# Performance work log

Hardware: AMD Instinct MI355X
Metric: run time of the kernel (lower is better)

The kernel has to match this reference:

```python
import jax, jax.numpy as jnp
import numpy as np

DIM = 1024
HEADS = 16
DHEAD = 64
INNER = HEADS * DHEAD
EPS = 1e-5


def layer_norm(x, g, b):
    mu = jnp.mean(x, axis=-1, keepdims=True)
    var = jnp.mean(jnp.square(x - mu), axis=-1, keepdims=True)
    return (x - mu) * jax.lax.rsqrt(var + EPS) * g + b


def apply_rope(x, cos, sin):
    # x: [b, h, s, d]; cos/sin broadcast as [1, 1, s, d/2]
    d2 = x.shape[-1] // 2
    x1, x2 = x[..., :d2], x[..., d2:]
    return jnp.concatenate([x1 * cos - x2 * sin, x2 * cos + x1 * sin], axis=-1)


def setup_inputs() -> dict:
    key = jax.random.key(0)
    ks = jax.random.split(key, 10)
    B, N, S = 8, 256, 4096
    latents = jax.random.normal(ks[0], (B, N, DIM), dtype=jnp.float32)
    context = jax.random.normal(ks[1], (B, S, DIM), dtype=jnp.float32)
    cos = jax.random.uniform(ks[2], (S, DHEAD // 2), dtype=jnp.float32)
    sin = jax.random.uniform(ks[3], (S, DHEAD // 2), dtype=jnp.float32)
    init = lambda k, shp, fan_in: jax.random.normal(k, shp, dtype=jnp.float32) / np.sqrt(fan_in)
    return {
        "latents": latents,
        "context": context,
        "cos": cos,
        "sin": sin,
        "ln_lat_g": jnp.ones((DIM,), jnp.float32),
        "ln_lat_b": jnp.zeros((DIM,), jnp.float32),
        "ln_ctx_g": jnp.ones((DIM,), jnp.float32),
        "ln_ctx_b": jnp.zeros((DIM,), jnp.float32),
        "Wq": init(ks[4], (DIM, INNER), DIM),
        "Wkv": init(ks[5], (DIM, 2 * INNER), DIM),
        "Wo": init(ks[6], (INNER, DIM), INNER),
        "bo": jnp.zeros((DIM,), jnp.float32),
    }


def reference(latents, context, cos, sin, ln_lat_g, ln_lat_b, ln_ctx_g, ln_ctx_b, Wq, Wkv, Wo, bo):
    b, n, _ = latents.shape
    s = context.shape[1]
    lat = layer_norm(latents, ln_lat_g, ln_lat_b)
    ctx = layer_norm(context, ln_ctx_g, ln_ctx_b)
    q = (lat @ Wq).reshape(b, n, HEADS, DHEAD).transpose(0, 2, 1, 3)   # [b,h,n,d]
    kv = ctx @ Wkv
    k, v = jnp.split(kv, 2, axis=-1)
    k = k.reshape(b, s, HEADS, DHEAD).transpose(0, 2, 1, 3)           # [b,h,s,d]
    v = v.reshape(b, s, HEADS, DHEAD).transpose(0, 2, 1, 3)
    k = apply_rope(k, cos[None, None], sin[None, None])
    scale = DHEAD ** (-0.5)
    attn = jnp.einsum('bhnd,bhsd->bhns', q, k) * scale
    attn = jnp.clip(attn, -11.0, 11.0)
    attn = jax.nn.softmax(attn, axis=-1)
    out = jnp.einsum('bhns,bhsd->bhnd', attn, v)
    out = out.transpose(0, 2, 1, 3).reshape(b, n, INNER)
    return out @ Wo + bo
```

## Files before the change

kernel.cpp:

```cpp
#include <hip/hip_runtime.h>
#include <hip/hip_bf16.h>
#include <math.h>

#define DIM   1024
#define HEADS 16
#define DHEAD 64
#define NB    8
#define NLAT  256
#define SCTX  4096

typedef short bf16x8 __attribute__((ext_vector_type(8)));
typedef float f32x4  __attribute__((ext_vector_type(4)));

__device__ __forceinline__ unsigned short f2b(float f) {
    union { float f; unsigned u; } x; x.f = f;
    unsigned r = x.u + 0x7FFFu + ((x.u >> 16) & 1u);
    return (unsigned short)(r >> 16);
}

__device__ __forceinline__ unsigned pkbf16(float a, float b) {
    float2 f2; f2.x = a; f2.y = b;
    __hip_bfloat162 h = __float22bfloat162_rn(f2);
    union { __hip_bfloat162 h; unsigned u; } cv; cv.h = h;
    return cv.u;
}

#define LN_WBLOCKS ((NB * NLAT + NB * SCTX) / 4)
__global__ __launch_bounds__(256) void prep_all(
    const float* __restrict__ latents, const float* __restrict__ context,
    const float* __restrict__ g_lat, const float* __restrict__ b_lat,
    const float* __restrict__ g_ctx, const float* __restrict__ b_ctx,
    const float* __restrict__ Wq, const float* __restrict__ Wkv,
    const float* __restrict__ Wo,
    unsigned short* __restrict__ lat_b, unsigned short* __restrict__ ctx_b,
    unsigned short* __restrict__ Wqb, unsigned short* __restrict__ Wkvb,
    unsigned short* __restrict__ Wob)
{
    int gb = blockIdx.x, t = threadIdx.x;
    if (gb < LN_WBLOCKS) {
        int wid = t >> 6, lane = t & 63;
        int row = gb * 4 + wid;
        const float* x; const float* g; const float* b; unsigned short* y; int r;
        if (row < NB * NLAT) { x = latents; g = g_lat; b = b_lat; y = lat_b; r = row; }
        else { x = context; g = g_ctx; b = b_ctx; y = ctx_b; r = row - NB * NLAT; }
        const float4* xr = (const float4*)(x + (size_t)r * DIM);
        float4 v[4];
        float s = 0.f, sq = 0.f;
        #pragma unroll
        for (int i = 0; i < 4; ++i) {
            v[i] = xr[lane + i * 64];
            s  += v[i].x + v[i].y + v[i].z + v[i].w;
            sq += v[i].x * v[i].x + v[i].y * v[i].y + v[i].z * v[i].z + v[i].w * v[i].w;
        }
        #pragma unroll
        for (int off = 32; off > 0; off >>= 1) {
            s  += __shfl_xor(s, off);
            sq += __shfl_xor(sq, off);
        }
        float mu = s * (1.0f / DIM);
        float rs = rsqrtf(sq * (1.0f / DIM) - mu * mu + 1e-5f);
        #pragma unroll
        for (int i = 0; i < 4; ++i) {
            float4 gg = ((const float4*)g)[lane + i * 64];
            float4 bb = ((const float4*)b)[lane + i * 64];
            ushort4 o;
            o.x = f2b((v[i].x - mu) * rs * gg.x + bb.x);
            o.y = f2b((v[i].y - mu) * rs * gg.y + bb.y);
            o.z = f2b((v[i].z - mu) * rs * gg.z + bb.z);
            o.w = f2b((v[i].w - mu) * rs * gg.w + bb.w);
            ((ushort4*)(y + (size_t)r * DIM))[lane + i * 64] = o;
        }
    } else {
        __shared__ unsigned short tile[32][33];
        int id = gb - LN_WBLOCKS;
        int z = id >> 10, y = (id >> 5) & 31, xb = id & 31;
        const float* W; unsigned short* Wt; int N, coloff = 0;
        switch (z) {
            case 0: W = Wq;  Wt = Wqb;  N = DIM;     break;
            case 1: W = Wkv; Wt = Wkvb; N = 2 * DIM; break;
            case 2: W = Wkv; Wt = Wkvb; N = 2 * DIM; coloff = DIM; break;
            default: W = Wo; Wt = Wob;  N = DIM;     break;
        }
        int n0 = xb * 32 + coloff, k0 = y * 32;
        int tx = t & 31, ty = t >> 5;
        #pragma unroll
        for (int i = 0; i < 4; ++i) {
            int k = k0 + ty + i * 8;
            tile[tx][ty + i * 8] = f2b(W[(size_t)k * N + n0 + tx]);
        }
        __syncthreads();
        #pragma unroll
        for (int i = 0; i < 4; ++i) {
            int n = n0 + ty + i * 8;
            Wt[(size_t)n * DIM + k0 + tx] = tile[ty + i * 8][tx];
        }
    }
}

__global__ __launch_bounds__(256, 2) void gemm_mfma(
    const unsigned short* __restrict__ A, const unsigned short* __restrict__ Bn,
    const unsigned short* __restrict__ Aq, const unsigned short* __restrict__ Bq,
    int K, const float* __restrict__ bias,
    const float* __restrict__ cosp, const float* __restrict__ sinp,
    float* __restrict__ outf,
    unsigned short* __restrict__ outk, unsigned short* __restrict__ outv,
    unsigned short* __restrict__ outq,
    int mode, int ldc)
{
    __shared__ __align__(16) unsigned short As[128 * 64];
    __shared__ __align__(16) unsigned short Bs[128 * 64];
    int t = threadIdx.x;
    int wave = t >> 6, lane = t & 63;
    int g = blockIdx.x;
    if (mode == 2) g += ldc;
    int m_tile, n_tile;
    if (mode == 2) {
        if (g >= 4096) {
            g -= 4096; mode = 1;
            A = Aq; Bn = Bq;
            n_tile = g & 7; m_tile = g >> 3;
        } else {
            int xcd = g & 7, j = g >> 3;
            int ngrp = j >> 8;
            n_tile = ngrp * 8 + (j & 7);
            m_tile = (xcd << 5) + ((j >> 3) & 31);
        }
    } else {
        n_tile = g & 7; m_tile = g >> 3;
    }
    int m_base = m_tile * 128, n_base = n_tile * 128;
    int wr = wave >> 1, wc = wave & 1;
    int quad = lane >> 4, ln = lane & 15;

    f32x4 zero = {0.f, 0.f, 0.f, 0.f};
    f32x4 acc[4][4];
    #pragma unroll
    for (int i = 0; i < 4; ++i)
        #pragma unroll
        for (int j = 0; j < 4; ++j) acc[i][j] = zero;

    const unsigned short* Ag = A  + (size_t)m_base * K;
    const unsigned short* Bg = Bn + (size_t)n_base * K;

    int srow  = lane >> 3;
    int schk  = ((lane & 7) ^ srow) * 8;

    for (int k0 = 0; k0 < K; k0 += 64) {
        __syncthreads();
        #pragma unroll
        for (int j = 0; j < 4; ++j) {
            int grp = j * 4 + wave;
            int row = grp * 8 + srow;
            __builtin_amdgcn_global_load_lds(
                (const __attribute__((address_space(1))) void*)(Ag + (size_t)row * K + k0 + schk),
                (__attribute__((address_space(3))) void*)(As + grp * 512 + lane * 8),
                16, 0, 0);
            __builtin_amdgcn_global_load_lds(
                (const __attribute__((address_space(1))) void*)(Bg + (size_t)row * K + k0 + schk),
                (__attribute__((address_space(3))) void*)(Bs + grp * 512 + lane * 8),
                16, 0, 0);
        }
        __syncthreads();
        #pragma unroll
        for (int kk = 0; kk < 2; ++kk) {
            bf16x8 af[4], bfr[4];
            int slot = ((kk * 4 + quad) ^ (ln & 7)) * 8;
            #pragma unroll
            for (int i = 0; i < 4; ++i) {
                af[i]  = *(const bf16x8*)(As + (wr * 64 + i * 16 + ln) * 64 + slot);
                bfr[i] = *(const bf16x8*)(Bs + (wc * 64 + i * 16 + ln) * 64 + slot);
            }
            #pragma unroll
            for (int i = 0; i < 4; ++i)
                #pragma unroll
                for (int j = 0; j < 4; ++j)
                    acc[i][j] = __builtin_amdgcn_mfma_f32_16x16x32_bf16(af[i], bfr[j], acc[i][j], 0, 0, 0);
        }
    }

    int cl = ln, rq = quad;
    if (mode == 2 && n_base >= DIM) {
        #pragma unroll
        for (int i = 0; i < 4; ++i) {
            int s0 = m_base + wr * 64 + i * 16 + rq * 4;
            int b  = s0 >> 12, s = s0 & 4095;
            #pragma unroll
            for (int j = 0; j < 4; ++j) {
                int n2 = n_base + wc * 64 + j * 16 + cl - DIM;
                int h = n2 >> 6, d = n2 & 63;
                ushort4 pk;
                pk.x = f2b(acc[i][j][0]); pk.y = f2b(acc[i][j][1]);
                pk.z = f2b(acc[i][j][2]); pk.w = f2b(acc[i][j][3]);
                *(ushort4*)(outv + (((size_t)(b * HEADS + h) * DHEAD + d) * SCTX) + s) = pk;
            }
        }
    } else if (mode == 2) {
        #pragma unroll
        for (int i = 0; i < 4; ++i) {
            #pragma unroll
            for (int r = 0; r < 4; ++r) {
                int m = m_base + wr * 64 + i * 16 + rq * 4 + r;
                int b = m >> 12, s = m & 4095;
                #pragma unroll
                for (int j = 0; j < 2; ++j) {
                    int n = n_base + wc * 64 + j * 16 + cl;
                    int h = n >> 6, d1 = n & 63;
                    float x1 = acc[i][j][r], x2 = acc[i][j + 2][r];
                    float c  = cosp[s * 32 + d1];
                    float sn = sinp[s * 32 + d1];
                    unsigned short* kr =
                        outk + (((size_t)(b * HEADS + h) * SCTX + s) * DHEAD) + d1;
                    kr[0]  = f2b(x1 * c - x2 * sn);
                    kr[32] = f2b(x2 * c + x1 * sn);
                }
            }
        }
    } else {
        #pragma unroll
        for (int i = 0; i < 4; ++i) {
            #pragma unroll
            for (int j = 0; j < 4; ++j) {
                #pragma unroll
                for (int r = 0; r < 4; ++r) {
                    int m = m_base + wr * 64 + i * 16 + rq * 4 + r;
                    int n = n_base + wc * 64 + j * 16 + cl;
                    float cv = acc[i][j][r];
                    if (mode == 0) {
                        outf[(size_t)m * ldc + n] = cv + bias[n];
                    } else {
                        int b = m >> 8, nn = m & 255;
                        int h = n >> 6, d = n & 63;
                        outq[(((size_t)(b * HEADS + h) * NLAT + nn) * DHEAD) + d] =
                            f2b(cv * 0.18033688f);
                    }
                }
            }
        }
    }
}

#define PPAD 72
#define CLIP2 15.8696454f

__global__ __launch_bounds__(256, 3) void attn_mfma(
    const unsigned short* __restrict__ qb,
    const unsigned short* __restrict__ kb,
    const unsigned short* __restrict__ vtb,
    float* __restrict__ accp,
    float* __restrict__ lp)
{
    __shared__ __align__(16) unsigned short Ks[2][64 * 64];
    __shared__ __align__(16) unsigned short Vs[2][64 * 64];
    __shared__ __align__(16) unsigned short Ps[4 * 32 * PPAD];

    int t = threadIdx.x, w = t >> 6, l = t & 63;
    int bx = blockIdx.x;
    int gg = ((bx >> 4) << 3) + (bx & 7);
    int qh = (bx >> 3) & 1;
    int bh = gg >> 2;
    int sh = gg & 3;
    int quad = l >> 4, ln = l & 15;
    int q0 = qh * 128 + w * 32;

    bf16x8 qf[2][2];
    const unsigned short* qbase = qb + ((size_t)bh * NLAT + q0) * DHEAD;
    #pragma unroll
    for (int qsub = 0; qsub < 2; ++qsub)
        #pragma unroll
        for (int kc = 0; kc < 2; ++kc)
            qf[qsub][kc] = *(const bf16x8*)(qbase + (qsub * 16 + ln) * DHEAD + kc * 32 + quad * 8);

    f32x4 acc[2][4];
    #pragma unroll
    for (int i = 0; i < 2; ++i)
        #pragma unroll
        for (int j = 0; j < 4; ++j) acc[i][j] = (f32x4){0.f, 0.f, 0.f, 0.f};
    float lacc[2] = {0.f, 0.f};

    const unsigned short* kgb = kb  + (size_t)bh * SCTX * DHEAD;
    const unsigned short* vgb = vtb + (size_t)bh * DHEAD * SCTX;
    unsigned short* Pw = Ps + w * 32 * PPAD;

    int srow8 = l >> 3;
    int csrc  = (l & 7) ^ srow8;

    auto STAGE = [&](int s0, int bi) {
        #pragma unroll
        for (int i = 0; i < 2; ++i) {
            int rbase = w * 8 + i * 32;
            int row = rbase + srow8;
            __builtin_amdgcn_global_load_lds(
                (const __attribute__((address_space(1))) void*)(kgb + (size_t)(s0 + row) * DHEAD + csrc * 8),
                (__attribute__((address_space(3))) void*)(&Ks[bi][rbase * 64] + (size_t)l * 8),
                16, 0, 0);
            __builtin_amdgcn_global_load_lds(
                (const __attribute__((address_space(1))) void*)(vgb + (size_t)row * SCTX + s0 + csrc * 8),
                (__attribute__((address_space(3))) void*)(&Vs[bi][rbase * 64] + (size_t)l * 8),
                16, 0, 0);
        }
    };

    const int s_begin = sh * 1024;
    const int NT = 1024 / 64;

    STAGE(s_begin, 0);
    __syncthreads();

    for (int it = 0; it < NT; ++it) {
        int buf = it & 1;
        if (it + 1 < NT)
            STAGE(s_begin + (it + 1) * 64, buf ^ 1);

        #pragma unroll
        for (int msub = 0; msub < 4; ++msub) {
            bf16x8 af[2];
            #pragma unroll
            for (int kc = 0; kc < 2; ++kc) {
                int sr = msub * 16 + ln;
                int ck = (4 * kc + quad) ^ (ln & 7);
                af[kc] = *(const bf16x8*)(&Ks[buf][sr * 64 + ck * 8]);
            }
            #pragma unroll
            for (int nsub = 0; nsub < 2; ++nsub) {
                f32x4 c = {0.f, 0.f, 0.f, 0.f};
                c = __builtin_amdgcn_mfma_f32_16x16x32_bf16(af[0], qf[nsub][0], c, 0, 0, 0);
                c = __builtin_amdgcn_mfma_f32_16x16x32_bf16(af[1], qf[nsub][1], c, 0, 0, 0);
                float p[4];
                #pragma unroll
                for (int r = 0; r < 4; ++r) {
                    float sc = __builtin_amdgcn_fmed3f(c[r], -CLIP2, CLIP2);
                    p[r] = __builtin_amdgcn_exp2f(sc - CLIP2);
                    lacc[nsub] += p[r];
                }
                uint2 pk;
                pk.x = pkbf16(p[0], p[1]);
                pk.y = pkbf16(p[2], p[3]);
                *(uint2*)(Pw + (nsub * 16 + ln) * PPAD + msub * 16 + quad * 4) = pk;
            }
        }
        #pragma unroll
        for (int kc = 0; kc < 2; ++kc) {
            bf16x8 pa[2];
            #pragma unroll
            for (int qsub = 0; qsub < 2; ++qsub)
                pa[qsub] = *(const bf16x8*)(Pw + (qsub * 16 + ln) * PPAD + kc * 32 + quad * 8);
            #pragma unroll
            for (int dsub = 0; dsub < 4; ++dsub) {
                int dr = dsub * 16 + ln;
                int ck = (4 * kc + quad) ^ (ln & 7);
                bf16x8 vb = *(const bf16x8*)(&Vs[buf][dr * 64 + ck * 8]);
                acc[0][dsub] = __builtin_amdgcn_mfma_f32_16x16x32_bf16(pa[0], vb, acc[0][dsub], 0, 0, 0);
                acc[1][dsub] = __builtin_amdgcn_mfma_f32_16x16x32_bf16(pa[1], vb, acc[1][dsub], 0, 0, 0);
            }
        }
        __syncthreads();
    }

    float* accs = accp + (size_t)sh * (NB * HEADS * NLAT * DHEAD);
    float* ls   = lp   + (size_t)sh * (NB * HEADS * NLAT);

    #pragma unroll
    for (int nsub = 0; nsub < 2; ++nsub) {
        float v = lacc[nsub];
        v += __shfl_xor(v, 16);
        v += __shfl_xor(v, 32);
        if (l < 16)
            ls[bh * NLAT + q0 + nsub * 16 + l] = v;
    }
    #pragma unroll
    for (int qsub = 0; qsub < 2; ++qsub)
        #pragma unroll
        for (int dsub = 0; dsub < 4; ++dsub)
            #pragma unroll
            for (int r = 0; r < 4; ++r) {
                int qg = q0 + qsub * 16 + quad * 4 + r;
                int dg = dsub * 16 + ln;
                accs[((size_t)bh * NLAT + qg) * DHEAD + dg] = acc[qsub][dsub][r];
            }
}

__global__ __launch_bounds__(256) void attn_finalize(
    const float* __restrict__ accp, const float* __restrict__ lp,
    unsigned short* __restrict__ aob)
{
    const int ACC = NB * HEADS * NLAT * DHEAD;
    const int LSZ = NB * HEADS * NLAT;
    int idx = blockIdx.x * 256 + threadIdx.x;
    int d = idx & 63;
    int rest = idx >> 6;
    int n = rest & 255, bh = rest >> 8;
    int b = bh >> 4, h = bh & 15;
    float a = accp[idx] + accp[idx + ACC] + accp[idx + 2 * ACC] + accp[idx + 3 * ACC];
    float l = lp[rest] + lp[rest + LSZ] + lp[rest + 2 * LSZ] + lp[rest + 3 * LSZ];
    aob[(((size_t)b * NLAT + n) * HEADS + h) * DHEAD + d] = f2b(a / l);
}

extern "C" void kernel_launch(void* const* d_in, const int* in_sizes, int n_in,
                              void* d_out, int out_size, void* d_ws, size_t ws_size,
                              hipStream_t stream) {
    const float* latents  = (const float*)d_in[0];
    const float* context  = (const float*)d_in[1];
    const float* cosp     = (const float*)d_in[2];
    const float* sinp     = (const float*)d_in[3];
    const float* ln_lat_g = (const float*)d_in[4];
    const float* ln_lat_b = (const float*)d_in[5];
    const float* ln_ctx_g = (const float*)d_in[6];
    const float* ln_ctx_b = (const float*)d_in[7];
    const float* Wq  = (const float*)d_in[8];
    const float* Wkv = (const float*)d_in[9];
    const float* Wo  = (const float*)d_in[10];
    const float* bo  = (const float*)d_in[11];
    float* out = (float*)d_out;

    char* base = (char*)d_ws;
    unsigned short* lat_b = (unsigned short*)(base + 0);
    unsigned short* ctx_b = (unsigned short*)(base + 4194304);
    unsigned short* Wqb   = (unsigned short*)(base + 71303168);
    unsigned short* Wkvb  = (unsigned short*)(base + 73400320);
    unsigned short* Wob   = (unsigned short*)(base + 77594624);
    unsigned short* q_b   = (unsigned short*)(base + 79691776);
    unsigned short* k_b   = (unsigned short*)(base + 83886080);
    unsigned short* vT_b  = (unsigned short*)(base + 150994944);
    float*          accp  = (float*)(base + 218103808);
    float*          lp    = (float*)(base + 251658240);
    unsigned short* aob   = (unsigned short*)(base + 252182528);

    hipLaunchKernelGGL(prep_all, dim3(LN_WBLOCKS + 4096), dim3(256), 0, stream,
                       latents, context, ln_lat_g, ln_lat_b, ln_ctx_g, ln_ctx_b,
                       Wq, Wkv, Wo, lat_b, ctx_b, Wqb, Wkvb, Wob);
    hipLaunchKernelGGL(gemm_mfma, dim3(1408), dim3(256), 0, stream,
                       ctx_b, Wkvb, lat_b, Wqb, DIM, (const float*)nullptr,
                       cosp, sinp,
                       (float*)nullptr, k_b, vT_b, q_b, 2, 0);
    hipLaunchKernelGGL(gemm_mfma, dim3(1408), dim3(256), 0, stream,
                       ctx_b, Wkvb, lat_b, Wqb, DIM, (const float*)nullptr,
                       cosp, sinp,
                       (float*)nullptr, k_b, vT_b, q_b, 2, 1408);
    hipLaunchKernelGGL(gemm_mfma, dim3(1408), dim3(256), 0, stream,
                       ctx_b, Wkvb, lat_b, Wqb, DIM, (const float*)nullptr,
                       cosp, sinp,
                       (float*)nullptr, k_b, vT_b, q_b, 2, 2816);
    hipLaunchKernelGGL(attn_mfma, dim3(NB * HEADS * 8), dim3(256), 0, stream,
                       q_b, k_b, vT_b, accp, lp);
    hipLaunchKernelGGL(attn_finalize, dim3(NB * HEADS * NLAT * DHEAD / 256), dim3(256), 0, stream,
                       accp, lp, aob);
    hipLaunchKernelGGL(gemm_mfma, dim3(128), dim3(256), 0, stream,
                       aob, Wob, (const unsigned short*)nullptr, (const unsigned short*)nullptr,
                       DIM, bo,
                       (const float*)nullptr, (const float*)nullptr,
                       out, (unsigned short*)nullptr, (unsigned short*)nullptr,
                       (unsigned short*)nullptr, 0, DIM);
}
```

Before: 507.5 us.

## Merge KV GEMM launches and process both query halves per attention block

The three split KV/Q projection GEMM launches become one launch of 4224 blocks, with a simpler XCD-aware tile mapping (16 n-tiles per m-group). The attention kernel now handles all 256 queries of a head/split in one block, so each K/V tile staged into LDS is reused across both query halves and total K/V global traffic is halved. The cost is twice the accumulator registers, with launch bounds lowered to 2 blocks per CU, and half as many attention blocks (512), which lowers parallelism.

```diff
diff --git a/kernel.cpp b/kernel.cpp
--- a/kernel.cpp
+++ b/kernel.cpp
@@ -112,7 +112,6 @@
     int t = threadIdx.x;
     int wave = t >> 6, lane = t & 63;
     int g = blockIdx.x;
-    if (mode == 2) g += ldc;
     int m_tile, n_tile;
     if (mode == 2) {
         if (g >= 4096) {
@@ -121,9 +120,8 @@
             n_tile = g & 7; m_tile = g >> 3;
         } else {
             int xcd = g & 7, j = g >> 3;
-            int ngrp = j >> 8;
-            n_tile = ngrp * 8 + (j & 7);
-            m_tile = (xcd << 5) + ((j >> 3) & 31);
+            n_tile = j & 15;
+            m_tile = (xcd << 5) + (j >> 4);
         }
     } else {
         n_tile = g & 7; m_tile = g >> 3;
@@ -242,7 +240,7 @@
 #define PPAD 72
 #define CLIP2 15.8696454f
 
-__global__ __launch_bounds__(256, 3) void attn_mfma(
+__global__ __launch_bounds__(256, 2) void attn_mfma(
     const unsigned short* __restrict__ qb,
     const unsigned short* __restrict__ kb,
     const unsigned short* __restrict__ vtb,
@@ -254,28 +252,30 @@
     __shared__ __align__(16) unsigned short Ps[4 * 32 * PPAD];
 
     int t = threadIdx.x, w = t >> 6, l = t & 63;
-    int bx = blockIdx.x;
-    int gg = ((bx >> 4) << 3) + (bx & 7);
-    int qh = (bx >> 3) & 1;
-    int bh = gg >> 2;
-    int sh = gg & 3;
+    int bh = blockIdx.x >> 2;
+    int sh = blockIdx.x & 3;
     int quad = l >> 4, ln = l & 15;
-    int q0 = qh * 128 + w * 32;
-
-    bf16x8 qf[2][2];
-    const unsigned short* qbase = qb + ((size_t)bh * NLAT + q0) * DHEAD;
+
+    bf16x8 qf[2][2][2];
     #pragma unroll
-    for (int qsub = 0; qsub < 2; ++qsub)
-        #pragma unroll
-        for (int kc = 0; kc < 2; ++kc)
-            qf[qsub][kc] = *(const bf16x8*)(qbase + (qsub * 16 + ln) * DHEAD + kc * 32 + quad * 8);
-
-    f32x4 acc[2][4];
+    for (int qblk = 0; qblk < 2; ++qblk) {
+        const unsigned short* qbase =
+            qb + ((size_t)bh * NLAT + qblk * 128 + w * 32) * DHEAD;
+        #pragma unroll
+        for (int qsub = 0; qsub < 2; ++qsub)
+            #pragma unroll
+            for (int kc = 0; kc < 2; ++kc)
+                qf[qblk][qsub][kc] = *(const bf16x8*)(qbase + (qsub * 16 + ln) * DHEAD + kc * 32 + quad * 8);
+    }
+
+    f32x4 acc[2][2][4];
     #pragma unroll
-    for (int i = 0; i < 2; ++i)
-        #pragma unroll
-        for (int j = 0; j < 4; ++j) acc[i][j] = (f32x4){0.f, 0.f, 0.f, 0.f};
-    float lacc[2] = {0.f, 0.f};
+    for (int qblk = 0; qblk < 2; ++qblk)
+        #pragma unroll
+        for (int i = 0; i < 2; ++i)
+            #pragma unroll
+            for (int j = 0; j < 4; ++j) acc[qblk][i][j] = (f32x4){0.f, 0.f, 0.f, 0.f};
+    float lacc[2][2] = {{0.f, 0.f}, {0.f, 0.f}};
 
     const unsigned short* kgb = kb  + (size_t)bh * SCTX * DHEAD;
     const unsigned short* vgb = vtb + (size_t)bh * DHEAD * SCTX;
@@ -312,45 +312,48 @@
             STAGE(s_begin + (it + 1) * 64, buf ^ 1);
 
         #pragma unroll
-        for (int msub = 0; msub < 4; ++msub) {
-            bf16x8 af[2];
+        for (int qblk = 0; qblk < 2; ++qblk) {
+            #pragma unroll
+            for (int msub = 0; msub < 4; ++msub) {
+                bf16x8 af[2];
+                #pragma unroll
+                for (int kc = 0; kc < 2; ++kc) {
+                    int sr = msub * 16 + ln;
+                    int ck = (4 * kc + quad) ^ (ln & 7);
+                    af[kc] = *(const bf16x8*)(&Ks[buf][sr * 64 + ck * 8]);
+                }
+                #pragma unroll
+                for (int nsub = 0; nsub < 2; ++nsub) {
+                    f32x4 c = {0.f, 0.f, 0.f, 0.f};
+                    c = __builtin_amdgcn_mfma_f32_16x16x32_bf16(af[0], qf[qblk][nsub][0], c, 0, 0, 0);
+                    c = __builtin_amdgcn_mfma_f32_16x16x32_bf16(af[1], qf[qblk][nsub][1], c, 0, 0, 0);
+                    float p[4];
+                    #pragma unroll
+                    for (int r = 0; r < 4; ++r) {
+                        float sc = __builtin_amdgcn_fmed3f(c[r], -CLIP2, CLIP2);
+                        p[r] = __builtin_amdgcn_exp2f(sc - CLIP2);
+                        lacc[qblk][nsub] += p[r];
+                    }
+                    uint2 pk;
+                    pk.x = pkbf16(p[0], p[1]);
+                    pk.y = pkbf16(p[2], p[3]);
+                    *(uint2*)(Pw + (nsub * 16 + ln) * PPAD + msub * 16 + quad * 4) = pk;
+                }
+            }
             #pragma unroll
             for (int kc = 0; kc < 2; ++kc) {
-                int sr = msub * 16 + ln;
-                int ck = (4 * kc + quad) ^ (ln & 7);
-                af[kc] = *(const bf16x8*)(&Ks[buf][sr * 64 + ck * 8]);
-            }
-            #pragma unroll
-            for (int nsub = 0; nsub < 2; ++nsub) {
-                f32x4 c = {0.f, 0.f, 0.f, 0.f};
-                c = __builtin_amdgcn_mfma_f32_16x16x32_bf16(af[0], qf[nsub][0], c, 0, 0, 0);
-                c = __builtin_amdgcn_mfma_f32_16x16x32_bf16(af[1], qf[nsub][1], c, 0, 0, 0);
-                float p[4];
-                #pragma unroll
-                for (int r = 0; r < 4; ++r) {
-                    float sc = __builtin_amdgcn_fmed3f(c[r], -CLIP2, CLIP2);
-                    p[r] = __builtin_amdgcn_exp2f(sc - CLIP2);
-                    lacc[nsub] += p[r];
-                }
-                uint2 pk;
-                pk.x = pkbf16(p[0], p[1]);
-                pk.y = pkbf16(p[2], p[3]);
-                *(uint2*)(Pw + (nsub * 16 + ln) * PPAD + msub * 16 + quad * 4) = pk;
-            }
-        }
-        #pragma unroll
-        for (int kc = 0; kc < 2; ++kc) {
-            bf16x8 pa[2];
-            #pragma unroll
-            for (int qsub = 0; qsub < 2; ++qsub)
-                pa[qsub] = *(const bf16x8*)(Pw + (qsub * 16 + ln) * PPAD + kc * 32 + quad * 8);
-            #pragma unroll
-            for (int dsub = 0; dsub < 4; ++dsub) {
-                int dr = dsub * 16 + ln;
-                int ck = (4 * kc + quad) ^ (ln & 7);
-                bf16x8 vb = *(const bf16x8*)(&Vs[buf][dr * 64 + ck * 8]);
-                acc[0][dsub] = __builtin_amdgcn_mfma_f32_16x16x32_bf16(pa[0], vb, acc[0][dsub], 0, 0, 0);
-                acc[1][dsub] = __builtin_amdgcn_mfma_f32_16x16x32_bf16(pa[1], vb, acc[1][dsub], 0, 0, 0);
+                bf16x8 pa[2];
+                #pragma unroll
+                for (int qsub = 0; qsub < 2; ++qsub)
+                    pa[qsub] = *(const bf16x8*)(Pw + (qsub * 16 + ln) * PPAD + kc * 32 + quad * 8);
+                #pragma unroll
+                for (int dsub = 0; dsub < 4; ++dsub) {
+                    int dr = dsub * 16 + ln;
+                    int ck = (4 * kc + quad) ^ (ln & 7);
+                    bf16x8 vb = *(const bf16x8*)(&Vs[buf][dr * 64 + ck * 8]);
+                    acc[qblk][0][dsub] = __builtin_amdgcn_mfma_f32_16x16x32_bf16(pa[0], vb, acc[qblk][0][dsub], 0, 0, 0);
+                    acc[qblk][1][dsub] = __builtin_amdgcn_mfma_f32_16x16x32_bf16(pa[1], vb, acc[qblk][1][dsub], 0, 0, 0);
+                }
             }
         }
         __syncthreads();
@@ -360,23 +363,27 @@
     float* ls   = lp   + (size_t)sh * (NB * HEADS * NLAT);
 
     #pragma unroll
-    for (int nsub = 0; nsub < 2; ++nsub) {
-        float v = lacc[nsub];
-        v += __shfl_xor(v, 16);
-        v += __shfl_xor(v, 32);
-        if (l < 16)
-            ls[bh * NLAT + q0 + nsub * 16 + l] = v;
-    }
+    for (int qblk = 0; qblk < 2; ++qblk)
+        #pragma unroll
+        for (int nsub = 0; nsub < 2; ++nsub) {
+            float v = lacc[qblk][nsub];
+            v += __shfl_xor(v, 16);
+            v += __shfl_xor(v, 32);
+            if (l < 16)
+                ls[bh * NLAT + qblk * 128 + w * 32 + nsub * 16 + l] = v;
+        }
     #pragma unroll
-    for (int qsub = 0; qsub < 2; ++qsub)
-        #pragma unroll
-        for (int dsub = 0; dsub < 4; ++dsub)
-            #pragma unroll
-            for (int r = 0; r < 4; ++r) {
-                int qg = q0 + qsub * 16 + quad * 4 + r;
-                int dg = dsub * 16 + ln;
-                accs[((size_t)bh * NLAT + qg) * DHEAD + dg] = acc[qsub][dsub][r];
-            }
+    for (int qblk = 0; qblk < 2; ++qblk)
+        #pragma unroll
+        for (int qsub = 0; qsub < 2; ++qsub)
+            #pragma unroll
+            for (int dsub = 0; dsub < 4; ++dsub)
+                #pragma unroll
+                for (int r = 0; r < 4; ++r) {
+                    int qg = qblk * 128 + w * 32 + qsub * 16 + quad * 4 + r;
+                    int dg = dsub * 16 + ln;
+                    accs[((size_t)bh * NLAT + qg) * DHEAD + dg] = acc[qblk][qsub][dsub][r];
+                }
 }
 
 __global__ __launch_bounds__(256) void attn_finalize(
@@ -428,19 +435,11 @@
     hipLaunchKernelGGL(prep_all, dim3(LN_WBLOCKS + 4096), dim3(256), 0, stream,
                        latents, context, ln_lat_g, ln_lat_b, ln_ctx_g, ln_ctx_b,
                        Wq, Wkv, Wo, lat_b, ctx_b, Wqb, Wkvb, Wob);
-    hipLaunchKernelGGL(gemm_mfma, dim3(1408), dim3(256), 0, stream,
+    hipLaunchKernelGGL(gemm_mfma, dim3(4096 + 128), dim3(256), 0, stream,
                        ctx_b, Wkvb, lat_b, Wqb, DIM, (const float*)nullptr,
                        cosp, sinp,
                        (float*)nullptr, k_b, vT_b, q_b, 2, 0);
-    hipLaunchKernelGGL(gemm_mfma, dim3(1408), dim3(256), 0, stream,
-                       ctx_b, Wkvb, lat_b, Wqb, DIM, (const float*)nullptr,
-                       cosp, sinp,
-                       (float*)nullptr, k_b, vT_b, q_b, 2, 1408);
-    hipLaunchKernelGGL(gemm_mfma, dim3(1408), dim3(256), 0, stream,
-                       ctx_b, Wkvb, lat_b, Wqb, DIM, (const float*)nullptr,
-                       cosp, sinp,
-                       (float*)nullptr, k_b, vT_b, q_b, 2, 2816);
-    hipLaunchKernelGGL(attn_mfma, dim3(NB * HEADS * 8), dim3(256), 0, stream,
+    hipLaunchKernelGGL(attn_mfma, dim3(NB * HEADS * 4), dim3(256), 0, stream,
                        q_b, k_b, vT_b, accp, lp);
     hipLaunchKernelGGL(attn_finalize, dim3(NB * HEADS * NLAT * DHEAD / 256), dim3(256), 0, stream,
                        accp, lp, aob);
```

New measurement: 488.7 us. 1.04x faster.
